# Kernel tuning notes

Measured on AMD Instinct MI355X. Metric: run time of the kernel, lower is better.

## Reference

```python
import jax, jax.numpy as jnp
import numpy as np

MATRIX_DIM = 128
FEAT = MATRIX_DIM * (MATRIX_DIM + 1) // 2  # 8256, triu incl. diagonal
HID = FEAT // 5                            # 1651
BATCH = 4096


def setup_inputs() -> dict:
    key = jax.random.key(0)
    k0, k1, k2, k3, k4 = jax.random.split(key, 5)
    stdv1 = 1.0 / FEAT / 2.0
    stdv2 = 1.0 / HID / 2.0
    return {
        "sim_matrices": jax.random.normal(k0, (BATCH, MATRIX_DIM, MATRIX_DIM), dtype=jnp.float32),
        "W1": jax.random.uniform(k1, (HID, FEAT), minval=-stdv1, maxval=stdv1, dtype=jnp.float32),
        "b1": jax.random.uniform(k2, (HID,), minval=-stdv1, maxval=stdv1, dtype=jnp.float32),
        "W2": jax.random.uniform(k3, (1, HID), minval=-stdv2, maxval=stdv2, dtype=jnp.float32),
        "b2": jax.random.uniform(k4, (1,), minval=-stdv2, maxval=stdv2, dtype=jnp.float32),
    }


def reference(sim_matrices, W1, b1, W2, b2):
    # flatten: take upper-triangular (incl. diag) entries -> [B, FEAT]
    iu0, iu1 = np.triu_indices(sim_matrices.shape[1])
    x = sim_matrices[:, iu0, iu1]
    # Linear_block 1 (ideal crossbar VMM = W x + b) + ReLU
    h = jax.nn.relu(jnp.einsum("bf,hf->bh", x, W1) + b1)
    # Linear_block 2 + Sigmoid -> [B, 1]
    return jax.nn.sigmoid(jnp.einsum("bh,oh->bo", h, W2) + b2)
```

## Files before the change

kernel.cpp:

```cpp
#include <hip/hip_runtime.h>
#include <hip/hip_bf16.h>
#include <math.h>

#define MDIM  128
#define FEAT  8256
#define HID   1651
#define HIDP  1664
#define BATCH 4096
#define BK    64
#define KT_TOTAL 129
#define NZ    2
#define KT_PER 64
#define W1SCALE 8192.0f
#define W1INV   (1.0f / 8192.0f)

using f32x4  = __attribute__((ext_vector_type(4))) float;
using bf16x8 = __attribute__((ext_vector_type(8))) __bf16;
typedef long long i64;

__device__ __forceinline__ void gload_lds16(const void* g, void* l) {
    __builtin_amdgcn_global_load_lds(
        (const __attribute__((address_space(1))) void*)g,
        (__attribute__((address_space(3))) void*)l,
        16, 0, 0);
}

__device__ __forceinline__ int row_off(int i) { return (i * (257 - i)) >> 1; }

__device__ __forceinline__ void pack8_fp8(const float* f, int* o) {
    int lo = __builtin_amdgcn_cvt_pk_fp8_f32(f[0], f[1], 0, false);
    lo     = __builtin_amdgcn_cvt_pk_fp8_f32(f[2], f[3], lo, true);
    int hi = __builtin_amdgcn_cvt_pk_fp8_f32(f[4], f[5], 0, false);
    hi     = __builtin_amdgcn_cvt_pk_fp8_f32(f[6], f[7], hi, true);
    o[0] = lo; o[1] = hi;
}

__global__ void __launch_bounds__(256)
pack_x_kernel(const float* __restrict__ sim, char* __restrict__ X) {
    const int b = blockIdx.x;
    const int t = threadIdx.x;
    const float* srow = sim + ((long long)b << 14);
    char* dst = X + (long long)b * FEAT;
#pragma unroll
    for (int it = 0; it < 5; ++it) {
        const int w = it * 256 + t;
        if (w < FEAT / 8) {
            const int f0 = w * 8;
            int i = (int)((257.0f - sqrtf(66049.0f - 8.0f * (float)f0)) * 0.5f);
            i = i < 0 ? 0 : (i > 127 ? 127 : i);
            while (i < 127 && row_off(i + 1) <= f0) ++i;
            while (i > 0 && row_off(i) > f0) --i;
            int j = i + (f0 - row_off(i));
            float v[8];
#pragma unroll
            for (int e = 0; e < 8; ++e) {
                if (j > 127) { ++i; j = i; }
                v[e] = srow[i * MDIM + j];
                ++j;
            }
            int o[2];
            pack8_fp8(v, o);
            *(int2*)(dst + f0) = make_int2(o[0], o[1]);
        }
    }
}

__global__ void __launch_bounds__(256)
conv_w1_kernel(const float* __restrict__ W1, char* __restrict__ W1p) {
    const int w = blockIdx.x * 256 + threadIdx.x;
    if (w >= FEAT / 8) return;
    const int n  = blockIdx.y;
    const int f0 = w * 8;
    int o[2];
    if (n < HID) {
        const float* src = W1 + (long long)n * FEAT + f0;
        const f32x4 a = *(const f32x4*)src;
        const f32x4 c = *(const f32x4*)(src + 4);
        float v[8];
#pragma unroll
        for (int e = 0; e < 4; ++e) {
            v[e]     = a[e] * W1SCALE;
            v[e + 4] = c[e] * W1SCALE;
        }
        pack8_fp8(v, o);
    } else {
        o[0] = 0; o[1] = 0;
    }
    *(int2*)(W1p + (long long)n * FEAT + f0) = make_int2(o[0], o[1]);
}

__global__ void __launch_bounds__(256, 4)
gemm_split_kernel(const char* __restrict__ X,
                  const char* __restrict__ W1p,
                  __hip_bfloat16* __restrict__ Cz) {
    __shared__ __align__(16) char lds_a[128 * BK];
    __shared__ __align__(16) char lds_b[128 * BK];

    const int t    = threadIdx.x;
    const int wave = t >> 6;
    const int lane = t & 63;
    const int bm   = blockIdx.x;
    const int bn   = blockIdx.y;
    const int z    = blockIdx.z;
    const int wm   = wave >> 1;
    const int wn   = wave & 1;
    const int lr   = lane & 15;
    const int lq   = lane >> 4;

    f32x4 acc[4][4];
#pragma unroll
    for (int i = 0; i < 4; ++i)
#pragma unroll
        for (int j = 0; j < 4; ++j)
            acc[i][j] = (f32x4){0.f, 0.f, 0.f, 0.f};

    const int kt0 = z * KT_PER;
    const int nkt = (z == NZ - 1) ? (KT_TOTAL - KT_PER * (NZ - 1)) : KT_PER;

    const int swst = (t & 3) ^ ((t >> 2) & 3) ^ ((t >> 4) & 3);
    const char* gA = X + (long long)(bm * 128 + (t >> 2)) * FEAT
                       + kt0 * BK + swst * 16;
    const char* gB = W1p + (long long)(bn * 128 + (t >> 2)) * FEAT
                         + kt0 * BK + swst * 16;
    char* lA = lds_a + wave * 1024;
    char* lB = lds_b + wave * 1024;

    const int ksw = (lq & 1) * 8;
    const int cl  = lq >> 1;

    for (int kt = 0; kt < nkt; ++kt) {
#pragma unroll
        for (int s = 0; s < 2; ++s) {
            gload_lds16(gA + (long long)s * 64 * FEAT, lA + s * 4096);
            gload_lds16(gB + (long long)s * 64 * FEAT, lB + s * 4096);
        }
        gA += BK;
        gB += BK;
        __syncthreads();

#pragma unroll
        for (int ks = 0; ks < 2; ++ks) {
            i64 av[4], bv[4];
#pragma unroll
            for (int i = 0; i < 4; ++i) {
                const int ra = wm * 64 + i * 16 + lr;
                const int rb = wn * 64 + i * 16 + lr;
                const int swa = (ra & 3) ^ ((ra >> 2) & 3);
                const int swb = (rb & 3) ^ ((rb >> 2) & 3);
                const int pa = ((ks * 2 + cl) ^ swa);
                const int pb = ((ks * 2 + cl) ^ swb);
                av[i] = *(const i64*)(lds_a + ra * 64 + pa * 16 + ksw);
                bv[i] = *(const i64*)(lds_b + rb * 64 + pb * 16 + ksw);
            }
#pragma unroll
            for (int i = 0; i < 4; ++i)
#pragma unroll
                for (int j = 0; j < 4; ++j)
                    acc[i][j] = __builtin_amdgcn_mfma_f32_16x16x32_fp8_fp8(
                        av[i], bv[j], acc[i][j], 0, 0, 0);
        }
        __syncthreads();
    }

    __hip_bfloat16* cz = Cz + ((long long)z * BATCH + bm * 128) * HIDP
                            + bn * 128 + wn * 64;
#pragma unroll
    for (int i = 0; i < 4; ++i)
#pragma unroll
        for (int r = 0; r < 4; ++r) {
            const int ml = wm * 64 + i * 16 + lq * 4 + r;
#pragma unroll
            for (int j = 0; j < 4; ++j)
                cz[(long long)ml * HIDP + j * 16 + lr] =
                    __float2bfloat16(acc[i][j][r]);
        }
}

__global__ void __launch_bounds__(256)
epilogue_kernel(const __hip_bfloat16* __restrict__ Cz,
                const float* __restrict__ b1,
                const float* __restrict__ W2,
                const float* __restrict__ b2,
                float* __restrict__ out) {
    const int b = blockIdx.x;
    const int t = threadIdx.x;
    float sum = 0.0f;
    const bf16x8* r0 = (const bf16x8*)(Cz + (long long)b * HIDP);
    const bf16x8* r1 = (const bf16x8*)(Cz + ((long long)BATCH + b) * HIDP);
    if (t < HIDP / 8) {
        const bf16x8 a = r0[t];
        const bf16x8 c = r1[t];
#pragma unroll
        for (int e = 0; e < 8; ++e) {
            const int n = t * 8 + e;
            if (n < HID) {
                const float v = ((float)a[e] + (float)c[e]) * W1INV + b1[n];
                sum += fmaxf(v, 0.0f) * W2[n];
            }
        }
    }
    sum += __shfl_xor(sum, 1);
    sum += __shfl_xor(sum, 2);
    sum += __shfl_xor(sum, 4);
    sum += __shfl_xor(sum, 8);
    sum += __shfl_xor(sum, 16);
    sum += __shfl_xor(sum, 32);
    __shared__ float wsum[4];
    if ((t & 63) == 0) wsum[t >> 6] = sum;
    __syncthreads();
    if (t == 0) {
        const float s = wsum[0] + wsum[1] + wsum[2] + wsum[3];
        out[b] = 1.0f / (1.0f + expf(-(s + b2[0])));
    }
}

extern "C" void kernel_launch(void* const* d_in, const int* in_sizes, int n_in,
                              void* d_out, int out_size, void* d_ws, size_t ws_size,
                              hipStream_t stream) {
    const float* sim = (const float*)d_in[0];
    const float* W1  = (const float*)d_in[1];
    const float* b1  = (const float*)d_in[2];
    const float* W2  = (const float*)d_in[3];
    const float* b2  = (const float*)d_in[4];
    float* out = (float*)d_out;

    char* ws = (char*)d_ws;
    const long long X_OFF   = 0;
    const long long W1P_OFF = (long long)BATCH * FEAT;
    const long long CZ_OFF  = W1P_OFF + (long long)HIDP * FEAT;
    char*           Xf8  = ws + X_OFF;
    char*           W1f8 = ws + W1P_OFF;
    __hip_bfloat16* Cz   = (__hip_bfloat16*)(ws + CZ_OFF);

    pack_x_kernel<<<BATCH, 256, 0, stream>>>(sim, Xf8);
    {
        dim3 grid((FEAT / 8 + 255) / 256, HIDP);
        conv_w1_kernel<<<grid, 256, 0, stream>>>(W1, W1f8);
    }
    {
        dim3 grid(BATCH / 128, HIDP / 128, NZ);
        gemm_split_kernel<<<grid, 256, 0, stream>>>(Xf8, W1f8, Cz);
    }
    epilogue_kernel<<<BATCH, 256, 0, stream>>>(Cz, b1, W2, b2, out);
}
```

Measured before the change: 504.4 us.

## Use 32x32x64 scaled fp8 MFMA with double-buffered LDS and fuse prep kernels

```diff
diff --git a/kernel.cpp b/kernel.cpp
--- a/kernel.cpp
+++ b/kernel.cpp
@@ -15,6 +15,9 @@
 #define W1INV   (1.0f / 8192.0f)
 
 using f32x4  = __attribute__((ext_vector_type(4))) float;
+using f32x16 = __attribute__((ext_vector_type(16))) float;
+using i32x4  = __attribute__((ext_vector_type(4))) int;
+using i32x8  = __attribute__((ext_vector_type(8))) int;
 using bf16x8 = __attribute__((ext_vector_type(8))) __bf16;
 typedef long long i64;
 
@@ -36,143 +39,155 @@
 }
 
 __global__ void __launch_bounds__(256)
-pack_x_kernel(const float* __restrict__ sim, char* __restrict__ X) {
-    const int b = blockIdx.x;
+prep_kernel(const float* __restrict__ sim, const float* __restrict__ W1,
+            char* __restrict__ X, char* __restrict__ W1p) {
     const int t = threadIdx.x;
-    const float* srow = sim + ((long long)b << 14);
-    char* dst = X + (long long)b * FEAT;
-#pragma unroll
-    for (int it = 0; it < 5; ++it) {
-        const int w = it * 256 + t;
-        if (w < FEAT / 8) {
-            const int f0 = w * 8;
-            int i = (int)((257.0f - sqrtf(66049.0f - 8.0f * (float)f0)) * 0.5f);
-            i = i < 0 ? 0 : (i > 127 ? 127 : i);
-            while (i < 127 && row_off(i + 1) <= f0) ++i;
-            while (i > 0 && row_off(i) > f0) --i;
-            int j = i + (f0 - row_off(i));
+    if (blockIdx.x < BATCH) {
+        const int b = blockIdx.x;
+        const float* srow = sim + ((i64)b << 14);
+        char* dst = X + (i64)b * FEAT;
+#pragma unroll
+        for (int it = 0; it < 5; ++it) {
+            const int w = it * 256 + t;
+            if (w < FEAT / 8) {
+                const int f0 = w * 8;
+                int i = (int)((257.0f - sqrtf(66049.0f - 8.0f * (float)f0)) * 0.5f);
+                i = i < 0 ? 0 : (i > 127 ? 127 : i);
+                while (i < 127 && row_off(i + 1) <= f0) ++i;
+                while (i > 0 && row_off(i) > f0) --i;
+                int j = i + (f0 - row_off(i));
+                float v[8];
+#pragma unroll
+                for (int e = 0; e < 8; ++e) {
+                    if (j > 127) { ++i; j = i; }
+                    v[e] = srow[i * MDIM + j];
+                    ++j;
+                }
+                int o[2];
+                pack8_fp8(v, o);
+                *(int2*)(dst + f0) = make_int2(o[0], o[1]);
+            }
+        }
+    } else {
+        const int c  = blockIdx.x - BATCH;
+        const int wb = c % 5;
+        const int n  = c / 5;
+        const int w  = wb * 256 + t;
+        if (w >= FEAT / 8) return;
+        const int f0 = w * 8;
+        int o[2];
+        if (n < HID) {
+            const float* src = W1 + (i64)n * FEAT + f0;
+            const f32x4 a = *(const f32x4*)src;
+            const f32x4 d = *(const f32x4*)(src + 4);
             float v[8];
 #pragma unroll
-            for (int e = 0; e < 8; ++e) {
-                if (j > 127) { ++i; j = i; }
-                v[e] = srow[i * MDIM + j];
-                ++j;
-            }
-            int o[2];
+            for (int e = 0; e < 4; ++e) {
+                v[e]     = a[e] * W1SCALE;
+                v[e + 4] = d[e] * W1SCALE;
+            }
             pack8_fp8(v, o);
-            *(int2*)(dst + f0) = make_int2(o[0], o[1]);
-        }
-    }
-}
-
-__global__ void __launch_bounds__(256)
-conv_w1_kernel(const float* __restrict__ W1, char* __restrict__ W1p) {
-    const int w = blockIdx.x * 256 + threadIdx.x;
-    if (w >= FEAT / 8) return;
-    const int n  = blockIdx.y;
-    const int f0 = w * 8;
-    int o[2];
-    if (n < HID) {
-        const float* src = W1 + (long long)n * FEAT + f0;
-        const f32x4 a = *(const f32x4*)src;
-        const f32x4 c = *(const f32x4*)(src + 4);
-        float v[8];
-#pragma unroll
-        for (int e = 0; e < 4; ++e) {
-            v[e]     = a[e] * W1SCALE;
-            v[e + 4] = c[e] * W1SCALE;
-        }
-        pack8_fp8(v, o);
-    } else {
-        o[0] = 0; o[1] = 0;
-    }
-    *(int2*)(W1p + (long long)n * FEAT + f0) = make_int2(o[0], o[1]);
+        } else {
+            o[0] = 0; o[1] = 0;
+        }
+        *(int2*)(W1p + (i64)n * FEAT + f0) = make_int2(o[0], o[1]);
+    }
 }
 
 __global__ void __launch_bounds__(256, 4)
 gemm_split_kernel(const char* __restrict__ X,
                   const char* __restrict__ W1p,
                   __hip_bfloat16* __restrict__ Cz) {
-    __shared__ __align__(16) char lds_a[128 * BK];
-    __shared__ __align__(16) char lds_b[128 * BK];
+    __shared__ __align__(16) char lds_a[2 * 8192];
+    __shared__ __align__(16) char lds_b[2 * 8192];
 
     const int t    = threadIdx.x;
-    const int wave = t >> 6;
-    const int lane = t & 63;
+    const int w    = t >> 6;
+    const int l    = t & 63;
     const int bm   = blockIdx.x;
     const int bn   = blockIdx.y;
     const int z    = blockIdx.z;
-    const int wm   = wave >> 1;
-    const int wn   = wave & 1;
-    const int lr   = lane & 15;
-    const int lq   = lane >> 4;
-
-    f32x4 acc[4][4];
-#pragma unroll
-    for (int i = 0; i < 4; ++i)
-#pragma unroll
-        for (int j = 0; j < 4; ++j)
-            acc[i][j] = (f32x4){0.f, 0.f, 0.f, 0.f};
+    const int wm   = w >> 1;
+    const int wn   = w & 1;
+    const int lm   = l & 31;
+    const int c0   = (l >> 5) << 1;
+
+    f32x16 acc[2][2];
+#pragma unroll
+    for (int r = 0; r < 16; ++r) {
+        acc[0][0][r] = 0.f; acc[0][1][r] = 0.f;
+        acc[1][0][r] = 0.f; acc[1][1][r] = 0.f;
+    }
 
     const int kt0 = z * KT_PER;
     const int nkt = (z == NZ - 1) ? (KT_TOTAL - KT_PER * (NZ - 1)) : KT_PER;
 
-    const int swst = (t & 3) ^ ((t >> 2) & 3) ^ ((t >> 4) & 3);
-    const char* gA = X + (long long)(bm * 128 + (t >> 2)) * FEAT
-                       + kt0 * BK + swst * 16;
-    const char* gB = W1p + (long long)(bn * 128 + (t >> 2)) * FEAT
-                         + kt0 * BK + swst * 16;
-    char* lA = lds_a + wave * 1024;
-    char* lB = lds_b + wave * 1024;
-
-    const int ksw = (lq & 1) * 8;
-    const int cl  = lq >> 1;
-
+    const int stR = ((w & 1) << 6) + l;
+    const int stC = w >> 1;
+    const char* gA0 = X + (i64)(bm * 128 + stR) * FEAT + kt0 * BK + stC * 16;
+    const char* gB0 = W1p + (i64)(bn * 128 + stR) * FEAT + kt0 * BK + stC * 16;
+    char* lA = lds_a + w * 1024;
+    char* lB = lds_b + w * 1024;
+
+#define STAGE(bufoff, kidx) do {                                   \
+        const char* _ga = gA0 + (i64)(kidx) * BK;                  \
+        const char* _gb = gB0 + (i64)(kidx) * BK;                  \
+        gload_lds16(_ga,      lA + (bufoff));                      \
+        gload_lds16(_ga + 32, lA + (bufoff) + 4096);               \
+        gload_lds16(_gb,      lB + (bufoff));                      \
+        gload_lds16(_gb + 32, lB + (bufoff) + 4096);               \
+    } while (0)
+
+    STAGE(0, 0);
+    __syncthreads();
+
+    int cur = 0;
     for (int kt = 0; kt < nkt; ++kt) {
-#pragma unroll
-        for (int s = 0; s < 2; ++s) {
-            gload_lds16(gA + (long long)s * 64 * FEAT, lA + s * 4096);
-            gload_lds16(gB + (long long)s * 64 * FEAT, lB + s * 4096);
-        }
-        gA += BK;
-        gB += BK;
+        const int nxt = cur ^ 1;
+        if (kt + 1 < nkt) STAGE(nxt * 8192, kt + 1);
+
+        const char* pa = lds_a + cur * 8192 + c0 * 2048 + (wm * 64 + lm) * 16;
+        const char* pb = lds_b + cur * 8192 + c0 * 2048 + (wn * 64 + lm) * 16;
+        const i32x4 a0l = *(const i32x4*)(pa);
+        const i32x4 a0h = *(const i32x4*)(pa + 2048);
+        const i32x4 a1l = *(const i32x4*)(pa + 512);
+        const i32x4 a1h = *(const i32x4*)(pa + 512 + 2048);
+        const i32x4 b0l = *(const i32x4*)(pb);
+        const i32x4 b0h = *(const i32x4*)(pb + 2048);
+        const i32x4 b1l = *(const i32x4*)(pb + 512);
+        const i32x4 b1h = *(const i32x4*)(pb + 512 + 2048);
+        const i32x8 A0 = __builtin_shufflevector(a0l, a0h, 0, 1, 2, 3, 4, 5, 6, 7);
+        const i32x8 A1 = __builtin_shufflevector(a1l, a1h, 0, 1, 2, 3, 4, 5, 6, 7);
+        const i32x8 B0 = __builtin_shufflevector(b0l, b0h, 0, 1, 2, 3, 4, 5, 6, 7);
+        const i32x8 B1 = __builtin_shufflevector(b1l, b1h, 0, 1, 2, 3, 4, 5, 6, 7);
+
+        acc[0][0] = __builtin_amdgcn_mfma_scale_f32_32x32x64_f8f6f4(
+            A0, B0, acc[0][0], 0, 0, 0, 0x7F7F7F7F, 0, 0x7F7F7F7F);
+        acc[0][1] = __builtin_amdgcn_mfma_scale_f32_32x32x64_f8f6f4(
+            A0, B1, acc[0][1], 0, 0, 0, 0x7F7F7F7F, 0, 0x7F7F7F7F);
+        acc[1][0] = __builtin_amdgcn_mfma_scale_f32_32x32x64_f8f6f4(
+            A1, B0, acc[1][0], 0, 0, 0, 0x7F7F7F7F, 0, 0x7F7F7F7F);
+        acc[1][1] = __builtin_amdgcn_mfma_scale_f32_32x32x64_f8f6f4(
+            A1, B1, acc[1][1], 0, 0, 0, 0x7F7F7F7F, 0, 0x7F7F7F7F);
+
         __syncthreads();
-
-#pragma unroll
-        for (int ks = 0; ks < 2; ++ks) {
-            i64 av[4], bv[4];
-#pragma unroll
-            for (int i = 0; i < 4; ++i) {
-                const int ra = wm * 64 + i * 16 + lr;
-                const int rb = wn * 64 + i * 16 + lr;
-                const int swa = (ra & 3) ^ ((ra >> 2) & 3);
-                const int swb = (rb & 3) ^ ((rb >> 2) & 3);
-                const int pa = ((ks * 2 + cl) ^ swa);
-                const int pb = ((ks * 2 + cl) ^ swb);
-                av[i] = *(const i64*)(lds_a + ra * 64 + pa * 16 + ksw);
-                bv[i] = *(const i64*)(lds_b + rb * 64 + pb * 16 + ksw);
-            }
-#pragma unroll
-            for (int i = 0; i < 4; ++i)
-#pragma unroll
-                for (int j = 0; j < 4; ++j)
-                    acc[i][j] = __builtin_amdgcn_mfma_f32_16x16x32_fp8_fp8(
-                        av[i], bv[j], acc[i][j], 0, 0, 0);
-        }
-        __syncthreads();
-    }
-
-    __hip_bfloat16* cz = Cz + ((long long)z * BATCH + bm * 128) * HIDP
+        cur = nxt;
+    }
+#undef STAGE
+
+    __hip_bfloat16* cz = Cz + ((i64)z * BATCH + bm * 128) * HIDP
                             + bn * 128 + wn * 64;
 #pragma unroll
-    for (int i = 0; i < 4; ++i)
-#pragma unroll
-        for (int r = 0; r < 4; ++r) {
-            const int ml = wm * 64 + i * 16 + lq * 4 + r;
-#pragma unroll
-            for (int j = 0; j < 4; ++j)
-                cz[(long long)ml * HIDP + j * 16 + lr] =
-                    __float2bfloat16(acc[i][j][r]);
+    for (int rb = 0; rb < 2; ++rb)
+#pragma unroll
+        for (int cb = 0; cb < 2; ++cb) {
+#pragma unroll
+            for (int reg = 0; reg < 16; ++reg) {
+                const int row = (reg & 3) + ((reg >> 2) << 3) + ((l >> 5) << 2);
+                const int ml  = wm * 64 + rb * 32 + row;
+                cz[(i64)ml * HIDP + cb * 32 + lm] =
+                    __float2bfloat16(acc[rb][cb][reg]);
+            }
         }
 }
 
@@ -185,8 +200,8 @@
     const int b = blockIdx.x;
     const int t = threadIdx.x;
     float sum = 0.0f;
-    const bf16x8* r0 = (const bf16x8*)(Cz + (long long)b * HIDP);
-    const bf16x8* r1 = (const bf16x8*)(Cz + ((long long)BATCH + b) * HIDP);
+    const bf16x8* r0 = (const bf16x8*)(Cz + (i64)b * HIDP);
+    const bf16x8* r1 = (const bf16x8*)(Cz + ((i64)BATCH + b) * HIDP);
     if (t < HIDP / 8) {
         const bf16x8 a = r0[t];
         const bf16x8 c = r1[t];
@@ -225,18 +240,14 @@
     float* out = (float*)d_out;
 
     char* ws = (char*)d_ws;
-    const long long X_OFF   = 0;
-    const long long W1P_OFF = (long long)BATCH * FEAT;
-    const long long CZ_OFF  = W1P_OFF + (long long)HIDP * FEAT;
+    const i64 X_OFF   = 0;
+    const i64 W1P_OFF = (i64)BATCH * FEAT;
+    const i64 CZ_OFF  = W1P_OFF + (i64)HIDP * FEAT;
     char*           Xf8  = ws + X_OFF;
     char*           W1f8 = ws + W1P_OFF;
     __hip_bfloat16* Cz   = (__hip_bfloat16*)(ws + CZ_OFF);
 
-    pack_x_kernel<<<BATCH, 256, 0, stream>>>(sim, Xf8);
-    {
-        dim3 grid((FEAT / 8 + 255) / 256, HIDP);
-        conv_w1_kernel<<<grid, 256, 0, stream>>>(W1, W1f8);
-    }
+    prep_kernel<<<BATCH + 5 * HIDP, 256, 0, stream>>>(sim, W1, Xf8, W1f8);
     {
         dim3 grid(BATCH / 128, HIDP / 128, NZ);
         gemm_split_kernel<<<grid, 256, 0, stream>>>(Xf8, W1f8, Cz);
```

Measured after the change: 525.8 us. 1.04x slower.
